# Kernel tuning notes

Measured on AMD Instinct MI355X. Metric: run time of the kernel, lower is better.

The kernel has to match this reference:

```python
import jax, jax.numpy as jnp
import numpy as np

N_GRAPHS = 100
NODES_PER_GRAPH = 1000
N = N_GRAPHS * NODES_PER_GRAPH
DEG = 16
E = N * DEG
IN_FEATS = 64
HIDDEN = 128
READOUT_DIM = HIDDEN // 2
SLOPE = 0.01
EPS = 1e-5


def leaky(x):
    return jnp.where(x >= 0, x, SLOPE * x)


def _kaiming(k, shape):
    # torch kaiming_uniform_, fan_in mode, leaky_relu gain
    fan_in = shape[0]
    gain = np.sqrt(2.0 / (1.0 + SLOPE ** 2))
    bound = gain * np.sqrt(3.0 / fan_in)
    return jax.random.uniform(k, shape, jnp.float32, -bound, bound)


def setup_inputs() -> dict:
    key = jax.random.key(0)
    ks = jax.random.split(key, 16)
    node_feats = jax.random.normal(ks[0], (N, IN_FEATS), jnp.float32)
    # within-graph random edges (batched graph of equal-sized components)
    src_local = jax.random.randint(ks[1], (E,), 0, NODES_PER_GRAPH)
    dst_local = jax.random.randint(ks[2], (E,), 0, NODES_PER_GRAPH)
    edge_graph = jnp.repeat(jnp.arange(N_GRAPHS, dtype=jnp.int32), E // N_GRAPHS)
    src = (edge_graph * NODES_PER_GRAPH + src_local).astype(jnp.int32)
    dst = (edge_graph * NODES_PER_GRAPH + dst_local).astype(jnp.int32)
    edge_weights = jax.random.uniform(ks[3], (E,), jnp.float32)
    node_graph = jnp.repeat(jnp.arange(N_GRAPHS, dtype=jnp.int32), NODES_PER_GRAPH)
    return {
        "node_feats": node_feats,
        "edge_weights": edge_weights,
        "W1": _kaiming(ks[4], (IN_FEATS, HIDDEN)),
        "W2": _kaiming(ks[5], (HIDDEN, HIDDEN)),
        "gn1_alpha": jnp.ones((HIDDEN,), jnp.float32),
        "gn1_gamma": jnp.ones((HIDDEN,), jnp.float32),
        "gn1_beta": jnp.zeros((HIDDEN,), jnp.float32),
        "gn2_alpha": jnp.ones((HIDDEN,), jnp.float32),
        "gn2_gamma": jnp.ones((HIDDEN,), jnp.float32),
        "gn2_beta": jnp.zeros((HIDDEN,), jnp.float32),
        "r1_w1": _kaiming(ks[6], (HIDDEN, HIDDEN)),
        "r1_b1": jnp.zeros((HIDDEN,), jnp.float32),
        "r1_w2": _kaiming(ks[7], (HIDDEN, READOUT_DIM)),
        "r1_b2": jnp.zeros((READOUT_DIM,), jnp.float32),
        "r2_w1": _kaiming(ks[8], (HIDDEN, HIDDEN)),
        "r2_b1": jnp.zeros((HIDDEN,), jnp.float32),
        "r2_w2": _kaiming(ks[9], (HIDDEN, READOUT_DIM)),
        "r2_b2": jnp.zeros((READOUT_DIM,), jnp.float32),
        "src": src,
        "dst": dst,
        "node_graph": node_graph,
    }


def _graph_conv(x, W, src, dst, ew, out_isqrt, in_isqrt):
    # DGL GraphConv norm='both', no bias: D_in^{-1/2} A_w D_out^{-1/2} X W
    h = (x * out_isqrt[:, None]) @ W                 # [N, out]
    m = h[src] * ew[:, None]                         # [E, out] gather + edge weight
    agg = jax.ops.segment_sum(m, dst, num_segments=N)  # scatter-add
    return agg * in_isqrt[:, None]


def _graph_norm(x, alpha, gamma, beta, node_graph, inv_cnt):
    mean = jax.ops.segment_sum(x, node_graph, num_segments=N_GRAPHS) * inv_cnt
    sub = x - alpha * mean[node_graph]
    var = jax.ops.segment_sum(sub * sub, node_graph, num_segments=N_GRAPHS) * inv_cnt
    return gamma * sub / jnp.sqrt(var[node_graph] + EPS) + beta


def _readout(x, w1, b1, w2, b2, node_graph, inv_cnt):
    # deep-sets style universal readout: rho(mean(phi(h_v)))
    h = leaky(x @ w1 + b1)
    pooled = jax.ops.segment_sum(h, node_graph, num_segments=N_GRAPHS) * inv_cnt
    return leaky(pooled @ w2 + b2)


def reference(node_feats, edge_weights, W1, W2,
              gn1_alpha, gn1_gamma, gn1_beta,
              gn2_alpha, gn2_gamma, gn2_beta,
              r1_w1, r1_b1, r1_w2, r1_b2,
              r2_w1, r2_b1, r2_w2, r2_b2,
              src, dst, node_graph):
    ones_e = jnp.ones((E,), jnp.float32)
    out_deg = jnp.clip(jax.ops.segment_sum(ones_e, src, num_segments=N), 1.0)
    in_deg = jnp.clip(jax.ops.segment_sum(ones_e, dst, num_segments=N), 1.0)
    out_isqrt = jax.lax.rsqrt(out_deg)
    in_isqrt = jax.lax.rsqrt(in_deg)
    inv_cnt = 1.0 / NODES_PER_GRAPH

    h = _graph_conv(node_feats, W1, src, dst, edge_weights, out_isqrt, in_isqrt)
    h = leaky(_graph_norm(h, gn1_alpha, gn1_gamma, gn1_beta, node_graph, inv_cnt))
    # dropout is identity in eval mode
    r1 = _readout(h, r1_w1, r1_b1, r1_w2, r1_b2, node_graph, inv_cnt)
    m1 = jax.ops.segment_sum(h, node_graph, num_segments=N_GRAPHS) * inv_cnt

    h = _graph_conv(h, W2, src, dst, edge_weights, out_isqrt, in_isqrt)
    h = leaky(_graph_norm(h, gn2_alpha, gn2_gamma, gn2_beta, node_graph, inv_cnt))
    r2 = _readout(h, r2_w1, r2_b1, r2_w2, r2_b2, node_graph, inv_cnt)
    m2 = jax.ops.segment_sum(h, node_graph, num_segments=N_GRAPHS) * inv_cnt

    readout = jnp.concatenate([r1, m1, r2, m2], axis=1)  # [G, 2*H + 2*H/2] = [100, 384]
    return leaky(readout)
```

## Files before the change

kernel.cpp:

```cpp
#include <hip/hip_runtime.h>
#include <cstddef>
#include <cstdint>

#define NG   100
#define NPG  1000
#define NN   (NG * NPG)
#define NE   (NN * 16)
#define EPG  (NE / NG)
#define CSRG 40000
#define MINREC 20
#define FIN  64
#define HID  128
#define RD   64
#define SLOPE 0.01f
#define EPSV  1e-5f
#define NSTRIP 250
#define GSN   40

using short8 = __attribute__((ext_vector_type(8))) short;
using f32x4  = __attribute__((ext_vector_type(4))) float;
typedef unsigned short u16;

__device__ __forceinline__ float leaky(float x) { return x >= 0.f ? x : SLOPE * x; }

__device__ __forceinline__ u16 f2bf(float f) {
  union { float f; unsigned u; } v; v.f = f;
  return (u16)((v.u + 0x7fffu + ((v.u >> 16) & 1u)) >> 16);
}
__device__ __forceinline__ float bf2f(u16 u) {
  union { unsigned u; float f; } v; v.u = ((unsigned)u) << 16;
  return v.f;
}

__device__ __forceinline__ bool swz(int b, int per_g, int& g, int& part) {
  const int xcd = b & 7;
  const int slot = b >> 3;
  g = xcd + 8 * (slot / per_g);
  part = slot % per_g;
  return g < NG;
}

struct BldSh { int hin[NPG]; int hout[NPG]; int cur[NPG]; int wtot[16]; };
struct GemSh { u16 Xl[64 * FIN]; u16 W[HID * FIN]; };
union FrontSh { BldSh b; GemSh g; };

__global__ __launch_bounds__(1024) void front_k(
    const float* __restrict__ X0, const float* __restrict__ ew,
    const int* __restrict__ src, const int* __restrict__ dst,
    const float* __restrict__ W1, const float* __restrict__ W2f,
    const float* __restrict__ R1f, const float* __restrict__ R2f,
    u16* __restrict__ Wt2, u16* __restrict__ Rt1, u16* __restrict__ Rt2,
    int* __restrict__ cin_, int* __restrict__ offs,
    unsigned* __restrict__ csr, u16* __restrict__ bufA,
    float* __restrict__ zeroreg) {
  __shared__ FrontSh u;
  const int b = blockIdx.x;
  const int t = threadIdx.x;
  if (b >= 208) {
    const int idx = (b - 208) * 1024 + t;
    if (idx < 3 * HID * HID) {
      const int m = idx >> 14, r = idx & 16383;
      const int n = r >> 7, k = r & 127;
      const float* s = (m == 0) ? W2f : (m == 1) ? R1f : R2f;
      u16* d = (m == 0) ? Wt2 : (m == 1) ? Rt1 : Rt2;
      d[r] = f2bf(s[k * HID + n]);
    }
    if (idx < (8 * NG * HID) / 4)
      ((float4*)zeroreg)[idx] = make_float4(0.f, 0.f, 0.f, 0.f);
    return;
  }
  int g, part;
  if (!swz(b, 2, g, part)) return;
  const int lane = t & 63, wave = t >> 6;
  const int nb = g * NPG, eb = g * EPG;

  if (part == 0) {
    if (t < NPG) { u.b.hin[t] = 0; u.b.hout[t] = 0; }
    __syncthreads();
    for (int e = t; e < EPG; e += 4096) {
      int s4[4], d4[4];
#pragma unroll
      for (int k = 0; k < 4; ++k) {
        const int ee = e + k * 1024;
        if (ee < EPG) { s4[k] = src[eb + ee]; d4[k] = dst[eb + ee]; }
        else d4[k] = -1;
      }
#pragma unroll
      for (int k = 0; k < 4; ++k)
        if (d4[k] >= 0) {
          atomicAdd(&u.b.hout[s4[k] - nb], 1);
          atomicAdd(&u.b.hin[d4[k] - nb], 1);
        }
    }
    __syncthreads();
    int v[4], vr[4];
    int loc = 0;
#pragma unroll
    for (int k = 0; k < 4; ++k) {
      const int idx = t * 4 + k;
      v[k] = (idx < NPG) ? u.b.hin[idx] : 0;
      const int c4 = (v[k] + 3) & ~3;
      vr[k] = (idx < NPG) ? ((c4 > MINREC) ? c4 : MINREC) : 0;
      loc += vr[k];
    }
    int incl = loc;
#pragma unroll
    for (int d = 1; d < 64; d <<= 1) {
      const int x = __shfl_up(incl, d);
      if (lane >= d) incl += x;
    }
    if (lane == 63) u.b.wtot[wave] = incl;
    if (t < NPG) cin_[nb + t] = u.b.hin[t];
    __syncthreads();
    float* houtf = (float*)u.b.hout;
    if (t < NPG) {
      const int c = u.b.hout[t];
      houtf[t] = rsqrtf((float)(c > 0 ? c : 1));
    }
    int wexc = 0;
    for (int i = 0; i < wave; ++i) wexc += u.b.wtot[i];
    int run = g * CSRG + wexc + (incl - loc);
#pragma unroll
    for (int k = 0; k < 4; ++k) {
      const int idx = t * 4 + k;
      if (idx < NPG) {
        offs[nb + idx] = run;
        u.b.cur[idx] = run;
        for (int z = v[k]; z < vr[k]; ++z) csr[run + z] = 0;
        run += vr[k];
      }
    }
    __syncthreads();
    for (int e = t; e < EPG; e += 4096) {
      int s4[4], d4[4];
      float w4[4];
#pragma unroll
      for (int k = 0; k < 4; ++k) {
        const int ee = e + k * 1024;
        if (ee < EPG) { s4[k] = src[eb + ee]; d4[k] = dst[eb + ee]; w4[k] = ew[eb + ee]; }
        else d4[k] = -1;
      }
#pragma unroll
      for (int k = 0; k < 4; ++k)
        if (d4[k] >= 0) {
          const int sl = s4[k] - nb;
          const int pos = atomicAdd(&u.b.cur[d4[k] - nb], 1);
          csr[pos] = ((unsigned)sl << 16) | (unsigned)f2bf(w4[k] * houtf[sl]);
        }
    }
  } else {
    const int l15 = lane & 15, quad = lane >> 4;
    const int rg = wave >> 2, cg = wave & 3;
    {
      const int n = t & 127, ko = t >> 7;
      short8 w8;
#pragma unroll
      for (int j = 0; j < 8; ++j) w8[j] = (short)f2bf(W1[(ko * 8 + j) * HID + n]);
      *(short8*)&u.g.W[n * FIN + ((ko ^ (n & 7)) << 3)] = w8;
    }
    const int kq = t & 15, srow = t >> 4;
    float4 xpre = (srow < NPG)
        ? *(const float4*)(X0 + (size_t)(nb + srow) * FIN + kq * 4)
        : make_float4(0.f, 0.f, 0.f, 0.f);
    for (int pass = 0; pass < 16; ++pass) {
      __syncthreads();
      {
        ushort4 uu = make_ushort4(f2bf(xpre.x), f2bf(xpre.y), f2bf(xpre.z), f2bf(xpre.w));
        const int cc = kq >> 1, half = kq & 1;
        *(ushort4*)&u.g.Xl[srow * FIN + (((cc ^ (srow & 7)) << 3) | (half << 2))] = uu;
      }
      __syncthreads();
      if (pass < 15) {
        const int rowi = (pass + 1) * 64 + srow;
        xpre = (rowi < NPG)
            ? *(const float4*)(X0 + (size_t)(nb + rowi) * FIN + kq * 4)
            : make_float4(0.f, 0.f, 0.f, 0.f);
      }
      short8 a[2];
      const int arow = rg * 16 + l15;
#pragma unroll
      for (int kt = 0; kt < 2; ++kt)
        a[kt] = *(const short8*)&u.g.Xl[arow * FIN + (((kt * 4 + quad) ^ (l15 & 7)) << 3)];
      int rows[4];
#pragma unroll
      for (int r = 0; r < 4; ++r) rows[r] = pass * 64 + rg * 16 + quad * 4 + r;
#pragma unroll
      for (int q2 = 0; q2 < 2; ++q2) {
        const int ct = cg * 2 + q2;
        f32x4 acc = {0.f, 0.f, 0.f, 0.f};
        const int brow = ct * 16 + l15;
#pragma unroll
        for (int kt = 0; kt < 2; ++kt) {
          const short8 bb = *(const short8*)&u.g.W[brow * FIN + (((kt * 4 + quad) ^ (l15 & 7)) << 3)];
          acc = __builtin_amdgcn_mfma_f32_16x16x32_bf16(a[kt], bb, acc, 0, 0, 0);
        }
        const int n2 = ct * 16 + l15;
#pragma unroll
        for (int r = 0; r < 4; ++r)
          if (rows[r] < NPG)
            bufA[(size_t)(nb + rows[r]) * HID + n2] = f2bf(acc[r]);
      }
    }
  }
}

__device__ __forceinline__ void norm_affine(const float* sx, const float* sq,
                                            const float* alpha, const float* gamma,
                                            const float* beta, int g, int c8,
                                            float* Av, float* Bv) {
  const float inv = 1.0f / NPG;
#pragma unroll
  for (int j = 0; j < 8; ++j) {
    const int f = c8 * 8 + j;
    const float mean = sx[g * HID + f] * inv;
    const float ex2 = sq[g * HID + f] * inv;
    const float am = alpha[f] * mean;
    const float var = fmaxf(ex2 - 2.0f * am * mean + am * am, 0.0f);
    const float A = gamma[f] * rsqrtf(var + EPSV);
    Av[j] = A;
    Bv[j] = beta[f] - A * am;
  }
}

__global__ __launch_bounds__(256) void gather_k(const u16* __restrict__ H,
                                                const unsigned* __restrict__ csr,
                                                const int* __restrict__ offs,
                                                const int* __restrict__ cin_,
                                                u16* __restrict__ AGG,
                                                float* __restrict__ sx,
                                                float* __restrict__ sq) {
  __shared__ float redx[4][HID];
  __shared__ float redq[4][HID];
  const int wave = threadIdx.x >> 6;
  const int lane = threadIdx.x & 63;
  int g, part;
  if (!swz(blockIdx.x, 25, g, part)) return;
  const int nb = g * NPG;
  const int base = nb + part * GSN;
  const int loff = lane * 2;
  const u16* __restrict__ Hg = H + (size_t)nb * HID;

  float sxa = 0.f, sxb = 0.f, sqa = 0.f, sqb = 0.f;
  for (int it = 0; it < 3; ++it) {
    const int nc = (it < 2) ? 4 : 2;
    int nn[4], cnt[4], c4p[4];
    float isq[4];
    const uint4* p[4];
#pragma unroll
    for (int c = 0; c < 4; ++c) {
      const int j = it * 4 + c;
      const int node = base + wave + ((j < 10) ? j : 0) * 4;
      nn[c] = node;
      const int nu = __builtin_amdgcn_readfirstlane(node);
      const int off = __builtin_amdgcn_readfirstlane(offs[nu]);
      cnt[c] = (c < nc) ? __builtin_amdgcn_readfirstlane(cin_[nu]) : 0;
      const int cr = (cnt[c] + 3) & ~3;
      c4p[c] = ((cr > MINREC) ? cr : MINREC) >> 2;
      isq[c] = rsqrtf(fmaxf((float)cnt[c], 1.0f));
      p[c] = (const uint4*)__builtin_assume_aligned(csr + off, 16);
    }
    float ax[4] = {0.f, 0.f, 0.f, 0.f};
    float ay[4] = {0.f, 0.f, 0.f, 0.f};
#pragma unroll
    for (int t = 0; t < 5; ++t) {
      unsigned rs[4][4];
#pragma unroll
      for (int c = 0; c < 4; ++c)
        if (c < nc) {
          const uint4 rv = p[c][t];
          rs[c][0] = __builtin_amdgcn_readfirstlane(rv.x);
          rs[c][1] = __builtin_amdgcn_readfirstlane(rv.y);
          rs[c][2] = __builtin_amdgcn_readfirstlane(rv.z);
          rs[c][3] = __builtin_amdgcn_readfirstlane(rv.w);
        }
      unsigned uu[4][4];
#pragma unroll
      for (int c = 0; c < 4; ++c)
        if (c < nc) {
#pragma unroll
          for (int q = 0; q < 4; ++q)
            uu[c][q] = ((const unsigned*)(Hg + (size_t)(rs[c][q] >> 16) * HID))[lane];
        }
#pragma unroll
      for (int c = 0; c < 4; ++c)
        if (c < nc) {
#pragma unroll
          for (int q = 0; q < 4; ++q) {
            const float w = bf2f((u16)(rs[c][q] & 0xffffu));
            ax[c] = fmaf(w, __uint_as_float(uu[c][q] << 16), ax[c]);
            ay[c] = fmaf(w, __uint_as_float(uu[c][q] & 0xffff0000u), ay[c]);
          }
        }
    }
#pragma unroll
    for (int c = 0; c < 4; ++c) {
      for (int t = 5; t < c4p[c]; ++t) {
        const uint4 rv = p[c][t];
        unsigned rsd[4];
        rsd[0] = __builtin_amdgcn_readfirstlane(rv.x);
        rsd[1] = __builtin_amdgcn_readfirstlane(rv.y);
        rsd[2] = __builtin_amdgcn_readfirstlane(rv.z);
        rsd[3] = __builtin_amdgcn_readfirstlane(rv.w);
#pragma unroll
        for (int q = 0; q < 4; ++q) {
          const unsigned uq = ((const unsigned*)(Hg + (size_t)(rsd[q] >> 16) * HID))[lane];
          const float w = bf2f((u16)(rsd[q] & 0xffffu));
          ax[c] = fmaf(w, __uint_as_float(uq << 16), ax[c]);
          ay[c] = fmaf(w, __uint_as_float(uq & 0xffff0000u), ay[c]);
        }
      }
    }
#pragma unroll
    for (int c = 0; c < 4; ++c)
      if (c < nc) {
        const float rx = ax[c] * isq[c];
        const float ry = ay[c] * isq[c];
        *(unsigned*)(AGG + (size_t)nn[c] * HID + loff) =
            (unsigned)f2bf(rx) | ((unsigned)f2bf(ry) << 16);
        sxa += rx; sxb += ry;
        sqa += rx * rx; sqb += ry * ry;
      }
  }
  redx[wave][loff] = sxa; redx[wave][loff + 1] = sxb;
  redq[wave][loff] = sqa; redq[wave][loff + 1] = sqb;
  __syncthreads();
  const int tid = threadIdx.x;
  if (tid < HID) {
    unsafeAtomicAdd(&sx[g * HID + tid],
                    redx[0][tid] + redx[1][tid] + redx[2][tid] + redx[3][tid]);
  } else {
    const int t = tid - HID;
    unsafeAtomicAdd(&sq[g * HID + t],
                    redq[0][t] + redq[1][t] + redq[2][t] + redq[3][t]);
  }
}

struct RedT { float red[16][HID]; float hred[16][HID]; };
union ShT { u16 Xl[64 * HID]; RedT r; };

template <bool DO_GEMM>
__global__ __launch_bounds__(256) void phigemm_k(const u16* __restrict__ Xb,
                                                 u16* __restrict__ Y,
                                                 const u16* __restrict__ Wt,
                                                 const u16* __restrict__ Rt,
                                                 const float* __restrict__ sx,
                                                 const float* __restrict__ sq,
                                                 const float* __restrict__ alpha,
                                                 const float* __restrict__ gamma,
                                                 const float* __restrict__ beta,
                                                 const float* __restrict__ b1,
                                                 float* __restrict__ phi_sum,
                                                 float* __restrict__ h_sum) {
  __shared__ ShT sh;
  __shared__ u16 Rl[HID * HID];
  __shared__ u16 Wl[DO_GEMM ? HID * HID : 8];
  const int tid = threadIdx.x;
  const int wave = tid >> 6, lane = tid & 63, l15 = lane & 15, quad = lane >> 4;
  int g, part;
  if (!swz(blockIdx.x, 4, g, part)) return;
  const int base = g * NPG + part * NSTRIP;
  const int c8 = tid & 15;
  const int srow = tid >> 4;

  for (int i = tid; i < HID * (HID / 8); i += 256) {
    const int n = i >> 4, c = i & 15;
    const short8 r2 = *(const short8*)(Rt + n * HID + c * 8);
    *(short8*)&Rl[n * HID + ((c ^ (n & 15)) << 3)] = r2;
    if (DO_GEMM) {
      const short8 w = *(const short8*)(Wt + n * HID + c * 8);
      *(short8*)&Wl[n * HID + ((c ^ (n & 15)) << 3)] = w;
    }
  }
  float Av[8], Bv[8];
  norm_affine(sx, sq, alpha, gamma, beta, g, c8, Av, Bv);
  float bcol[8];
#pragma unroll
  for (int ct = 0; ct < 8; ++ct) bcol[ct] = b1[ct * 16 + l15];

  float pooled[8] = {0.f, 0.f, 0.f, 0.f, 0.f, 0.f, 0.f, 0.f};
  float hp[8] = {0.f, 0.f, 0.f, 0.f, 0.f, 0.f, 0.f, 0.f};
  const short8 z8 = {0, 0, 0, 0, 0, 0, 0, 0};
  short8 xpre[4];
#pragma unroll
  for (int it = 0; it < 4; ++it) {
    const int rowi = srow + it * 16;
    xpre[it] = (rowi < NSTRIP) ? *(const short8*)(Xb + (size_t)(base + rowi) * HID + c8 * 8) : z8;
  }
  for (int pass = 0; pass < 4; ++pass) {
    __syncthreads();
#pragma unroll
    for (int it = 0; it < 4; ++it) {
      const int r = srow + it * 16;
      const int rowi = pass * 64 + r;
      short8 o = z8;
      if (rowi < NSTRIP) {
#pragma unroll
        for (int j = 0; j < 8; ++j) {
          const float xn = leaky(fmaf(Av[j], bf2f((u16)xpre[it][j]), Bv[j]));
          hp[j] += xn;
          o[j] = (short)f2bf(xn);
        }
      }
      *(short8*)&sh.Xl[r * HID + ((c8 ^ (r & 15)) << 3)] = o;
    }
    __syncthreads();
    if (pass < 3) {
#pragma unroll
      for (int it = 0; it < 4; ++it) {
        const int rowi = (pass + 1) * 64 + srow + it * 16;
        xpre[it] = (rowi < NSTRIP) ? *(const short8*)(Xb + (size_t)(base + rowi) * HID + c8 * 8) : z8;
      }
    }
    short8 a[4];
    const int arow = wave * 16 + l15;
#pragma unroll
    for (int kt = 0; kt < 4; ++kt)
      a[kt] = *(const short8*)&sh.Xl[arow * HID + (((kt * 4 + quad) ^ l15) << 3)];
    int rows[4];
#pragma unroll
    for (int r = 0; r < 4; ++r) rows[r] = pass * 64 + wave * 16 + quad * 4 + r;
#pragma unroll
    for (int ct = 0; ct < 8; ++ct) {
      const int brow = ct * 16 + l15;
      if (DO_GEMM) {
        f32x4 accW = {0.f, 0.f, 0.f, 0.f};
#pragma unroll
        for (int kt = 0; kt < 4; ++kt) {
          const short8 bb = *(const short8*)&Wl[brow * HID + (((kt * 4 + quad) ^ l15) << 3)];
          accW = __builtin_amdgcn_mfma_f32_16x16x32_bf16(a[kt], bb, accW, 0, 0, 0);
        }
#pragma unroll
        for (int r = 0; r < 4; ++r)
          if (rows[r] < NSTRIP)
            Y[(size_t)(base + rows[r]) * HID + ct * 16 + l15] = f2bf(accW[r]);
      }
      f32x4 accR = {0.f, 0.f, 0.f, 0.f};
#pragma unroll
      for (int kt = 0; kt < 4; ++kt) {
        const short8 bb = *(const short8*)&Rl[brow * HID + (((kt * 4 + quad) ^ l15) << 3)];
        accR = __builtin_amdgcn_mfma_f32_16x16x32_bf16(a[kt], bb, accR, 0, 0, 0);
      }
#pragma unroll
      for (int r = 0; r < 4; ++r)
        if (rows[r] < NSTRIP) pooled[ct] += leaky(accR[r] + bcol[ct]);
    }
  }
  __syncthreads();
  const int qi = wave * 4 + quad;
#pragma unroll
  for (int ct = 0; ct < 8; ++ct) sh.r.red[qi][ct * 16 + l15] = pooled[ct];
#pragma unroll
  for (int j = 0; j < 8; ++j) sh.r.hred[tid >> 4][(tid & 15) * 8 + j] = hp[j];
  __syncthreads();
  if (tid < HID) {
    float s = 0.f;
#pragma unroll
    for (int q = 0; q < 16; ++q) s += sh.r.red[q][tid];
    unsafeAtomicAdd(&phi_sum[g * HID + tid], s);
  } else {
    const int t = tid - HID;
    float s = 0.f;
#pragma unroll
    for (int rr = 0; rr < 16; ++rr) s += sh.r.hred[rr][t];
    unsafeAtomicAdd(&h_sum[g * HID + t], s);
  }
}

__global__ __launch_bounds__(64) void fin_k(const float* __restrict__ ps1,
                                            const float* __restrict__ hs1,
                                            const float* __restrict__ ps2,
                                            const float* __restrict__ hs2,
                                            const float* __restrict__ r1w2,
                                            const float* __restrict__ r1b2,
                                            const float* __restrict__ r2w2,
                                            const float* __restrict__ r2b2,
                                            float* __restrict__ out) {
  const int gb = blockIdx.x;
  const bool L2 = gb >= NG;
  const int g = L2 ? gb - NG : gb;
  const float* ps = L2 ? ps2 : ps1;
  const float* hs = L2 ? hs2 : hs1;
  const float* w2 = L2 ? r2w2 : r1w2;
  const float* b2 = L2 ? r2b2 : r1b2;
  const int roff = L2 ? 192 : 0;
  const int moff = L2 ? 256 : 64;
  const int j = threadIdx.x;
  float acc = b2[j];
#pragma unroll 8
  for (int k = 0; k < HID; ++k)
    acc += (ps[g * HID + k] * (1.0f / NPG)) * w2[k * RD + j];
  out[g * 384 + roff + j] = leaky(leaky(acc));
  out[g * 384 + moff + j] = leaky(hs[g * HID + j] * (1.0f / NPG));
  out[g * 384 + moff + 64 + j] = leaky(hs[g * HID + 64 + j] * (1.0f / NPG));
}

extern "C" void kernel_launch(void* const* d_in, const int* in_sizes, int n_in,
                              void* d_out, int out_size, void* d_ws, size_t ws_size,
                              hipStream_t stream) {
  const float* node_feats = (const float*)d_in[0];
  const float* ew   = (const float*)d_in[1];
  const float* W1   = (const float*)d_in[2];
  const float* W2   = (const float*)d_in[3];
  const float* g1a  = (const float*)d_in[4];
  const float* g1g  = (const float*)d_in[5];
  const float* g1b  = (const float*)d_in[6];
  const float* g2a  = (const float*)d_in[7];
  const float* g2g  = (const float*)d_in[8];
  const float* g2b  = (const float*)d_in[9];
  const float* r1w1 = (const float*)d_in[10];
  const float* r1b1 = (const float*)d_in[11];
  const float* r1w2 = (const float*)d_in[12];
  const float* r1b2 = (const float*)d_in[13];
  const float* r2w1 = (const float*)d_in[14];
  const float* r2b1 = (const float*)d_in[15];
  const float* r2w2 = (const float*)d_in[16];
  const float* r2b2 = (const float*)d_in[17];
  const int* src = (const int*)d_in[18];
  const int* dst = (const int*)d_in[19];
  float* out = (float*)d_out;

  char* wsb = (char*)d_ws;
  float* ps1     = (float*)wsb;
  float* hs1     = ps1 + NG * HID;
  float* ps2     = hs1 + NG * HID;
  float* hs2     = ps2 + NG * HID;
  float* sx1     = hs2 + NG * HID;
  float* sq1     = sx1 + NG * HID;
  float* sx2     = sq1 + NG * HID;
  float* sq2     = sx2 + NG * HID;
  int*   cin     = (int*)(sq2 + NG * HID);
  int*   offs    = cin + NN;
  unsigned* csr  = (unsigned*)(offs + NN);
  u16*   Wt2     = (u16*)(csr + (size_t)NG * CSRG);
  u16*   Rt1     = Wt2 + HID * HID;
  u16*   Rt2     = Rt1 + HID * HID;
  u16*   bufA    = Rt2 + HID * HID;
  u16*   bufB    = bufA + (size_t)NN * HID;

  const int gemm_grid = 8 * 4 * 13;
  const int gather_grid = 8 * 25 * 13;

  front_k<<<208 + 56, 1024, 0, stream>>>(node_feats, ew, src, dst,
                                         W1, W2, r1w1, r2w1,
                                         Wt2, Rt1, Rt2,
                                         cin, offs, csr, bufA, ps1);

  gather_k<<<gather_grid, 256, 0, stream>>>(bufA, csr, offs, cin, bufB, sx1, sq1);
  phigemm_k<true><<<gemm_grid, 256, 0, stream>>>(bufB, bufA, Wt2, Rt1,
                                                 sx1, sq1, g1a, g1g, g1b,
                                                 r1b1, ps1, hs1);

  gather_k<<<gather_grid, 256, 0, stream>>>(bufA, csr, offs, cin, bufB, sx2, sq2);
  phigemm_k<false><<<gemm_grid, 256, 0, stream>>>(bufB, nullptr, nullptr, Rt2,
                                                  sx2, sq2, g2a, g2g, g2b,
                                                  r2b1, ps2, hs2);

  fin_k<<<2 * NG, 64, 0, stream>>>(ps1, hs1, ps2, hs2, r1w2, r1b2, r2w2, r2b2, out);
}
```

Measured before the change: 269.3 us.

## Build CSR in shared memory and read GEMM weights directly from global

The CSR builder now scatters edges into a per-graph LDS buffer of 24000 entries and then copies it to global memory with coalesced uint4 stores. This replaces the zero-fill plus random scattered global writes and shrinks the per-graph stride. Separately, phigemm no longer stages the W and R weight matrices in LDS and loads MFMA B operands straight from global/L2, which cuts LDS use and staging time and may raise occupancy, at the cost of uncoalesced global reads. Edges whose position exceeds the 24000-entry LDS capacity are silently dropped, which is a correctness risk if padded row sizes ever overflow it.

```diff
diff --git a/kernel.cpp b/kernel.cpp
--- a/kernel.cpp
+++ b/kernel.cpp
@@ -7,7 +7,7 @@
 #define NN   (NG * NPG)
 #define NE   (NN * 16)
 #define EPG  (NE / NG)
-#define CSRG 40000
+#define CSRL 24000
 #define MINREC 20
 #define FIN  64
 #define HID  128
@@ -40,7 +40,14 @@
   return g < NG;
 }
 
-struct BldSh { int hin[NPG]; int hout[NPG]; int cur[NPG]; int wtot[16]; };
+struct BldSh {
+  unsigned csrl[CSRL];
+  int hin[NPG];
+  int hout[NPG];
+  int cur[NPG];
+  int wtot[16];
+  int total;
+};
 struct GemSh { u16 Xl[64 * FIN]; u16 W[HID * FIN]; };
 union FrontSh { BldSh b; GemSh g; };
 
@@ -75,6 +82,15 @@
   const int nb = g * NPG, eb = g * EPG;
 
   if (part == 0) {
+    {
+      const uint4 z4 = {0u, 0u, 0u, 0u};
+      uint4* c4 = (uint4*)u.b.csrl;
+#pragma unroll
+      for (int i = 0; i < CSRL / 4 / 1024 + 1; ++i) {
+        const int j = t + i * 1024;
+        if (j < CSRL / 4) c4[j] = z4;
+      }
+    }
     if (t < NPG) { u.b.hin[t] = 0; u.b.hout[t] = 0; }
     __syncthreads();
     for (int e = t; e < EPG; e += 4096) {
@@ -119,15 +135,15 @@
     }
     int wexc = 0;
     for (int i = 0; i < wave; ++i) wexc += u.b.wtot[i];
-    int run = g * CSRG + wexc + (incl - loc);
+    int run = wexc + (incl - loc);
 #pragma unroll
     for (int k = 0; k < 4; ++k) {
       const int idx = t * 4 + k;
       if (idx < NPG) {
-        offs[nb + idx] = run;
+        offs[nb + idx] = g * CSRL + run;
         u.b.cur[idx] = run;
-        for (int z = v[k]; z < vr[k]; ++z) csr[run + z] = 0;
         run += vr[k];
+        if (idx == NPG - 1) u.b.total = run;
       }
     }
     __syncthreads();
@@ -145,8 +161,16 @@
         if (d4[k] >= 0) {
           const int sl = s4[k] - nb;
           const int pos = atomicAdd(&u.b.cur[d4[k] - nb], 1);
-          csr[pos] = ((unsigned)sl << 16) | (unsigned)f2bf(w4[k] * houtf[sl]);
-        }
+          if (pos < CSRL)
+            u.b.csrl[pos] = ((unsigned)sl << 16) | (unsigned)f2bf(w4[k] * houtf[sl]);
+        }
+    }
+    __syncthreads();
+    {
+      const int tot4 = (u.b.total + 3) >> 2;
+      const uint4* s4p = (const uint4*)u.b.csrl;
+      uint4* d4p = (uint4*)(csr + (size_t)g * CSRL);
+      for (int i = t; i < tot4; i += 1024) d4p[i] = s4p[i];
     }
   } else {
     const int l15 = lane & 15, quad = lane >> 4;
@@ -352,8 +376,6 @@
                                                  float* __restrict__ phi_sum,
                                                  float* __restrict__ h_sum) {
   __shared__ ShT sh;
-  __shared__ u16 Rl[HID * HID];
-  __shared__ u16 Wl[DO_GEMM ? HID * HID : 8];
   const int tid = threadIdx.x;
   const int wave = tid >> 6, lane = tid & 63, l15 = lane & 15, quad = lane >> 4;
   int g, part;
@@ -362,15 +384,6 @@
   const int c8 = tid & 15;
   const int srow = tid >> 4;
 
-  for (int i = tid; i < HID * (HID / 8); i += 256) {
-    const int n = i >> 4, c = i & 15;
-    const short8 r2 = *(const short8*)(Rt + n * HID + c * 8);
-    *(short8*)&Rl[n * HID + ((c ^ (n & 15)) << 3)] = r2;
-    if (DO_GEMM) {
-      const short8 w = *(const short8*)(Wt + n * HID + c * 8);
-      *(short8*)&Wl[n * HID + ((c ^ (n & 15)) << 3)] = w;
-    }
-  }
   float Av[8], Bv[8];
   norm_affine(sx, sq, alpha, gamma, beta, g, c8, Av, Bv);
   float bcol[8];
@@ -426,7 +439,7 @@
         f32x4 accW = {0.f, 0.f, 0.f, 0.f};
 #pragma unroll
         for (int kt = 0; kt < 4; ++kt) {
-          const short8 bb = *(const short8*)&Wl[brow * HID + (((kt * 4 + quad) ^ l15) << 3)];
+          const short8 bb = *(const short8*)(Wt + (size_t)brow * HID + (kt * 4 + quad) * 8);
           accW = __builtin_amdgcn_mfma_f32_16x16x32_bf16(a[kt], bb, accW, 0, 0, 0);
         }
 #pragma unroll
@@ -437,7 +450,7 @@
       f32x4 accR = {0.f, 0.f, 0.f, 0.f};
 #pragma unroll
       for (int kt = 0; kt < 4; ++kt) {
-        const short8 bb = *(const short8*)&Rl[brow * HID + (((kt * 4 + quad) ^ l15) << 3)];
+        const short8 bb = *(const short8*)(Rt + (size_t)brow * HID + (kt * 4 + quad) * 8);
         accR = __builtin_amdgcn_mfma_f32_16x16x32_bf16(a[kt], bb, accR, 0, 0, 0);
       }
 #pragma unroll
@@ -531,7 +544,7 @@
   int*   cin     = (int*)(sq2 + NG * HID);
   int*   offs    = cin + NN;
   unsigned* csr  = (unsigned*)(offs + NN);
-  u16*   Wt2     = (u16*)(csr + (size_t)NG * CSRG);
+  u16*   Wt2     = (u16*)(csr + (size_t)NG * CSRL);
   u16*   Rt1     = Wt2 + HID * HID;
   u16*   Rt2     = Rt1 + HID * HID;
   u16*   bufA    = Rt2 + HID * HID;
```

After: 299.4 us. +11.2%, slower.
